# Kernel tuning notes

Measured on AMD Instinct MI355X. Metric: run time of the kernel, lower is better.

The kernel has to match this reference:

```python
import jax, jax.numpy as jnp
import numpy as np

PREV_SIZE = 1024
SIZE = 4096
BATCH = 8192


def setup_inputs() -> dict:
    key = jax.random.key(0)
    k1, k2, k3, k4 = jax.random.split(key, 4)
    return {
        "prev_layer_output": jax.random.normal(k1, (PREV_SIZE, BATCH), dtype=jnp.float32),
        "input_A_weights": jax.random.normal(k2, (SIZE, PREV_SIZE), dtype=jnp.float32),
        "input_B_weights": jax.random.normal(k3, (SIZE, PREV_SIZE), dtype=jnp.float32),
        "table_weights": jax.random.normal(k4, (16, SIZE), dtype=jnp.float32),
    }


def reference(prev_layer_output, input_A_weights, input_B_weights, table_weights):
    # Soft input selection via row-softmax over previous neurons.
    pa = jax.nn.softmax(input_A_weights, axis=1)   # (size, prev_size)
    pb = jax.nn.softmax(input_B_weights, axis=1)   # (size, prev_size)
    pt = jax.nn.softmax(table_weights, axis=0)     # (16, size) softmax over gates

    A = pa @ prev_layer_output                     # (size, batch)
    B = pb @ prev_layer_output                     # (size, batch)
    AB = A * B

    p = pt[:, :, None]                             # (16, size, 1) broadcast over batch
    # Fused weighted sum over the 16 soft logic gates (no (16,size,batch) buffer).
    out = (
        p[1] * AB
        + p[2] * (A - AB)
        + p[3] * A
        + p[4] * (B - AB)
        + p[5] * B
        + p[6] * (A + B - 2.0 * AB)
        + p[7] * (A + B - AB)
        + p[8] * (1.0 - (A + B - AB))
        + p[9] * (1.0 - (A + B - 2.0 * AB))
        + p[10] * (1.0 - B)
        + p[11] * (1.0 - B + AB)
        + p[12] * (1.0 - A)
        + p[13] * (1.0 - A + AB)
        + p[14] * (1.0 - AB)
        + p[15]
    )
    return out
```

## Files before the change

kernel.cpp:

```cpp
#include <hip/hip_runtime.h>
#include <hip/hip_bf16.h>

#define K_DIM 1024
#define M_DIM 4096
#define N_DIM 8192
#define BK 32
#define BM 128
#define BN 128
#define NT 32

#define OFF_A 0
#define OFF_B 8192
#define OFF_P 16384
#define BUF_BYTES 24576

typedef __attribute__((ext_vector_type(8))) __bf16 bf16x8_t;
typedef __attribute__((ext_vector_type(4))) float f32x4;

#define SBAR __builtin_amdgcn_s_barrier()
#define VMCNT0 asm volatile("s_waitcnt vmcnt(0)" ::: "memory")

__device__ inline unsigned short f2bf(float f) {
    unsigned u = __float_as_uint(f);
    u += 0x7FFF + ((u >> 16) & 1);
    return (unsigned short)(u >> 16);
}

__device__ __forceinline__ void gload_lds16(const void* g, void* l) {
    __builtin_amdgcn_global_load_lds(
        (const __attribute__((address_space(1))) unsigned int*)g,
        (__attribute__((address_space(3))) unsigned int*)l, 16, 0, 0);
}

__global__ void dual_softmax_kernel(const float* __restrict__ wa,
                                    const float* __restrict__ wb,
                                    unsigned short* __restrict__ pa,
                                    unsigned short* __restrict__ pb) {
    const int idx = blockIdx.x;
    const float* w = (idx < M_DIM) ? wa : wb;
    unsigned short* o = (idx < M_DIM) ? pa : pb;
    const int row = idx & (M_DIM - 1);
    const int tid = threadIdx.x;
    const float4 v = reinterpret_cast<const float4*>(w + (size_t)row * K_DIM)[tid];
    float m = fmaxf(fmaxf(v.x, v.y), fmaxf(v.z, v.w));
    #pragma unroll
    for (int off = 32; off >= 1; off >>= 1) m = fmaxf(m, __shfl_xor(m, off));
    __shared__ float redm[4];
    __shared__ float reds[4];
    if ((tid & 63) == 0) redm[tid >> 6] = m;
    __syncthreads();
    m = fmaxf(fmaxf(redm[0], redm[1]), fmaxf(redm[2], redm[3]));
    const float e0 = __expf(v.x - m), e1 = __expf(v.y - m);
    const float e2 = __expf(v.z - m), e3 = __expf(v.w - m);
    float s = e0 + e1 + e2 + e3;
    #pragma unroll
    for (int off = 32; off >= 1; off >>= 1) s += __shfl_xor(s, off);
    if ((tid & 63) == 0) reds[tid >> 6] = s;
    __syncthreads();
    s = reds[0] + reds[1] + reds[2] + reds[3];
    const float inv = 1.0f / s;
    ushort4 r;
    r.x = f2bf(e0 * inv); r.y = f2bf(e1 * inv);
    r.z = f2bf(e2 * inv); r.w = f2bf(e3 * inv);
    reinterpret_cast<ushort4*>(o + (size_t)row * K_DIM)[tid] = r;
}

__global__ void transpose_conv_kernel(const float* __restrict__ src,
                                      unsigned short* __restrict__ dst) {
    __shared__ float t[32][33];
    const int n0 = blockIdx.x * 32;
    const int k0 = blockIdx.y * 32;
    const int tx = threadIdx.x, ty = threadIdx.y;
    #pragma unroll
    for (int i = ty; i < 32; i += 8)
        t[i][tx] = src[(size_t)(k0 + i) * N_DIM + n0 + tx];
    __syncthreads();
    #pragma unroll
    for (int i = ty; i < 32; i += 8)
        dst[(size_t)(n0 + i) * K_DIM + k0 + tx] = f2bf(t[tx][i]);
}

__global__ void coef_kernel(const float* __restrict__ tw,
                            float4* __restrict__ coef) {
    const int r = blockIdx.x * 256 + threadIdx.x;
    float p[16];
    float m = -1e30f;
    #pragma unroll
    for (int k = 0; k < 16; ++k) { p[k] = tw[k * M_DIM + r]; m = fmaxf(m, p[k]); }
    float s = 0.f;
    #pragma unroll
    for (int k = 0; k < 16; ++k) { p[k] = __expf(p[k] - m); s += p[k]; }
    const float inv = 1.f / s;
    #pragma unroll
    for (int k = 0; k < 16; ++k) p[k] *= inv;
    const float cA  = p[2]+p[3]+p[6]+p[7]-p[8]-p[9]-p[12]-p[13];
    const float cB  = p[4]+p[5]+p[6]+p[7]-p[8]-p[9]-p[10]-p[11];
    const float cAB = p[1]-p[2]-p[4]-2.f*p[6]-p[7]+p[8]+2.f*p[9]+p[11]+p[13]-p[14];
    const float c0  = p[8]+p[9]+p[10]+p[11]+p[12]+p[13]+p[14]+p[15];
    coef[r] = make_float4(cA, cB, cAB, c0);
}

__global__ __launch_bounds__(256, 2)
void dual_gemm_kernel(const unsigned short* __restrict__ pa,
                      const unsigned short* __restrict__ pb,
                      const unsigned short* __restrict__ pv,
                      const float4* __restrict__ coef,
                      float* __restrict__ out) {
    __shared__ unsigned short lds[2 * BUF_BYTES / 2];

    const int tid = threadIdx.x;
    const int lane = tid & 63;
    const int w = tid >> 6;
    const int wm = w >> 1, wn = w & 1;
    const int bm = blockIdx.y, bn = blockIdx.x;

    const int sub  = lane >> 2;
    const int scol = (lane & 3) ^ ((lane >> 3) & 3);

    const int c0 = 2 * w, c1 = 2 * w + 1;
    const char* sA0 = (const char*)pa + ((size_t)(bm * BM + c0 * 16 + sub) * K_DIM) * 2 + scol * 16;
    const char* sA1 = (const char*)pa + ((size_t)(bm * BM + c1 * 16 + sub) * K_DIM) * 2 + scol * 16;
    const char* sB0 = (const char*)pb + ((size_t)(bm * BM + c0 * 16 + sub) * K_DIM) * 2 + scol * 16;
    const char* sB1 = (const char*)pb + ((size_t)(bm * BM + c1 * 16 + sub) * K_DIM) * 2 + scol * 16;
    const char* sP0 = (const char*)pv + ((size_t)(bn * BN + c0 * 16 + sub) * K_DIM) * 2 + scol * 16;
    const char* sP1 = (const char*)pv + ((size_t)(bn * BN + c1 * 16 + sub) * K_DIM) * 2 + scol * 16;

    const int fr = lane & 15;
    const int fk = lane >> 4;

    int aoff[4], poff[4];
    #pragma unroll
    for (int i = 0; i < 4; ++i) {
        const int ar = wm * 64 + fr + i * 16;
        aoff[i] = ar * 64 + ((fk ^ ((ar >> 1) & 3)) << 4);
        const int pr = wn * 64 + fr + i * 16;
        poff[i] = pr * 64 + ((fk ^ ((pr >> 1) & 3)) << 4);
    }

    f32x4 accA[4][4], accB[4][4];
    const f32x4 z = {0.f, 0.f, 0.f, 0.f};
    #pragma unroll
    for (int i = 0; i < 4; ++i)
        #pragma unroll
        for (int j = 0; j < 4; ++j) { accA[i][j] = z; accB[i][j] = z; }

    #define STAGE_TO(buf_base) do {                                          \
        char* base = (char*)(buf_base);                                      \
        gload_lds16(sA0, base + OFF_A + c0 * 1024);                          \
        gload_lds16(sA1, base + OFF_A + c1 * 1024);                          \
        gload_lds16(sB0, base + OFF_B + c0 * 1024);                          \
        gload_lds16(sB1, base + OFF_B + c1 * 1024);                          \
        gload_lds16(sP0, base + OFF_P + c0 * 1024);                          \
        gload_lds16(sP1, base + OFF_P + c1 * 1024);                          \
        sA0 += BK * 2; sA1 += BK * 2; sB0 += BK * 2; sB1 += BK * 2;          \
        sP0 += BK * 2; sP1 += BK * 2;                                        \
    } while (0)

    char* buf0 = (char*)lds;
    char* buf1 = (char*)lds + BUF_BYTES;

    STAGE_TO(buf0);
    VMCNT0;
    SBAR;

    for (int t = 0; t < NT; ++t) {
        const bool more = (t < NT - 1);
        if (more) STAGE_TO(buf1);

        bf16x8_t af[4], bfv[4], pf[4];
        #pragma unroll
        for (int i = 0; i < 4; ++i) {
            af[i]  = *reinterpret_cast<const bf16x8_t*>(buf0 + OFF_A + aoff[i]);
            bfv[i] = *reinterpret_cast<const bf16x8_t*>(buf0 + OFF_B + aoff[i]);
            pf[i]  = *reinterpret_cast<const bf16x8_t*>(buf0 + OFF_P + poff[i]);
        }

        __builtin_amdgcn_s_setprio(1);
        #pragma unroll
        for (int mi = 0; mi < 4; ++mi)
            #pragma unroll
            for (int ni = 0; ni < 4; ++ni) {
                accA[mi][ni] = __builtin_amdgcn_mfma_f32_16x16x32_bf16(
                    af[mi], pf[ni], accA[mi][ni], 0, 0, 0);
                accB[mi][ni] = __builtin_amdgcn_mfma_f32_16x16x32_bf16(
                    bfv[mi], pf[ni], accB[mi][ni], 0, 0, 0);
            }
        __builtin_amdgcn_s_setprio(0);

        if (more) {
            VMCNT0;
            SBAR;
        }
        char* tmp = buf0; buf0 = buf1; buf1 = tmp;
    }

    const int row_grp = lane >> 4;
    #pragma unroll
    for (int mi = 0; mi < 4; ++mi) {
        #pragma unroll
        for (int ni = 0; ni < 4; ++ni) {
            const int gr0 = bm * BM + wm * 64 + mi * 16 + row_grp * 4;
            const int gc  = bn * BN + wn * 64 + ni * 16 + (lane & 15);
            #pragma unroll
            for (int i = 0; i < 4; ++i) {
                const int r = gr0 + i;
                const float4 cf = coef[r];
                const float av = accA[mi][ni][i];
                const float bv = accB[mi][ni][i];
                out[(size_t)r * N_DIM + gc] =
                    fmaf(cf.z, av * bv, fmaf(cf.x, av, fmaf(cf.y, bv, cf.w)));
            }
        }
    }
}

extern "C" void kernel_launch(void* const* d_in, const int* in_sizes, int n_in,
                              void* d_out, int out_size, void* d_ws, size_t ws_size,
                              hipStream_t stream) {
    const float* prev = (const float*)d_in[0];
    const float* wa   = (const float*)d_in[1];
    const float* wb   = (const float*)d_in[2];
    const float* tw   = (const float*)d_in[3];
    float* out = (float*)d_out;

    char* ws = (char*)d_ws;
    unsigned short* pa = (unsigned short*)ws;
    unsigned short* pb = (unsigned short*)(ws + 8388608);
    unsigned short* pv = (unsigned short*)(ws + 16777216);
    float4* coef       = (float4*)(ws + 33554432);

    dual_softmax_kernel<<<2 * M_DIM, 256, 0, stream>>>(wa, wb, pa, pb);
    transpose_conv_kernel<<<dim3(N_DIM / 32, K_DIM / 32), dim3(32, 8), 0, stream>>>(prev, pv);
    coef_kernel<<<M_DIM / 256, 256, 0, stream>>>(tw, coef);
    dual_gemm_kernel<<<dim3(N_DIM / BN, M_DIM / BM), 256, 0, stream>>>(pa, pb, pv, coef, out);
}
```

Baseline: 164.0 us.

## Load A/B softmax operands directly from global into registers, stage only P in LDS

The A and B weight tiles are no longer staged through LDS. Each wave instead loads its own rows straight from global memory into registers, double-buffered, and only the shared prev-layer tile goes through LDS. This shrinks LDS use from 48KB to 16KB per block and removes LDS read traffic for A/B. The cost is that wm-paired waves load A/B redundantly from global/L2 with less coalesced 16-byte row accesses, and register pressure rises from the extra fragment buffers.

```diff
diff --git a/kernel.cpp b/kernel.cpp
--- a/kernel.cpp
+++ b/kernel.cpp
@@ -9,10 +9,7 @@
 #define BN 128
 #define NT 32
 
-#define OFF_A 0
-#define OFF_B 8192
-#define OFF_P 16384
-#define BUF_BYTES 24576
+#define PBUF_BYTES 8192
 
 typedef __attribute__((ext_vector_type(8))) __bf16 bf16x8_t;
 typedef __attribute__((ext_vector_type(4))) float f32x4;
@@ -106,7 +103,7 @@
                       const unsigned short* __restrict__ pv,
                       const float4* __restrict__ coef,
                       float* __restrict__ out) {
-    __shared__ unsigned short lds[2 * BUF_BYTES / 2];
+    __shared__ unsigned short lds[2 * PBUF_BYTES / 2];
 
     const int tid = threadIdx.x;
     const int lane = tid & 63;
@@ -116,25 +113,22 @@
 
     const int sub  = lane >> 2;
     const int scol = (lane & 3) ^ ((lane >> 3) & 3);
-
     const int c0 = 2 * w, c1 = 2 * w + 1;
-    const char* sA0 = (const char*)pa + ((size_t)(bm * BM + c0 * 16 + sub) * K_DIM) * 2 + scol * 16;
-    const char* sA1 = (const char*)pa + ((size_t)(bm * BM + c1 * 16 + sub) * K_DIM) * 2 + scol * 16;
-    const char* sB0 = (const char*)pb + ((size_t)(bm * BM + c0 * 16 + sub) * K_DIM) * 2 + scol * 16;
-    const char* sB1 = (const char*)pb + ((size_t)(bm * BM + c1 * 16 + sub) * K_DIM) * 2 + scol * 16;
     const char* sP0 = (const char*)pv + ((size_t)(bn * BN + c0 * 16 + sub) * K_DIM) * 2 + scol * 16;
     const char* sP1 = (const char*)pv + ((size_t)(bn * BN + c1 * 16 + sub) * K_DIM) * 2 + scol * 16;
 
+    const unsigned short* gA = pa +
+        (size_t)(bm * BM + wm * 64 + (lane & 15)) * K_DIM + (lane >> 4) * 8;
+    const unsigned short* gB = pb +
+        (size_t)(bm * BM + wm * 64 + (lane & 15)) * K_DIM + (lane >> 4) * 8;
+
     const int fr = lane & 15;
     const int fk = lane >> 4;
-
-    int aoff[4], poff[4];
-    #pragma unroll
-    for (int i = 0; i < 4; ++i) {
-        const int ar = wm * 64 + fr + i * 16;
-        aoff[i] = ar * 64 + ((fk ^ ((ar >> 1) & 3)) << 4);
-        const int pr = wn * 64 + fr + i * 16;
-        poff[i] = pr * 64 + ((fk ^ ((pr >> 1) & 3)) << 4);
+    int poff[4];
+    #pragma unroll
+    for (int ni = 0; ni < 4; ++ni) {
+        const int pr = wn * 64 + fr + ni * 16;
+        poff[ni] = pr * 64 + ((fk ^ ((pr >> 1) & 3)) << 4);
     }
 
     f32x4 accA[4][4], accB[4][4];
@@ -144,55 +138,69 @@
         #pragma unroll
         for (int j = 0; j < 4; ++j) { accA[i][j] = z; accB[i][j] = z; }
 
-    #define STAGE_TO(buf_base) do {                                          \
-        char* base = (char*)(buf_base);                                      \
-        gload_lds16(sA0, base + OFF_A + c0 * 1024);                          \
-        gload_lds16(sA1, base + OFF_A + c1 * 1024);                          \
-        gload_lds16(sB0, base + OFF_B + c0 * 1024);                          \
-        gload_lds16(sB1, base + OFF_B + c1 * 1024);                          \
-        gload_lds16(sP0, base + OFF_P + c0 * 1024);                          \
-        gload_lds16(sP1, base + OFF_P + c1 * 1024);                          \
-        sA0 += BK * 2; sA1 += BK * 2; sB0 += BK * 2; sB1 += BK * 2;          \
+    char* const buf0 = (char*)lds;
+    char* const buf1 = (char*)lds + PBUF_BYTES;
+
+    #define STAGE_P(base) do {                                               \
+        gload_lds16(sP0, (base) + c0 * 1024);                                \
+        gload_lds16(sP1, (base) + c1 * 1024);                                \
         sP0 += BK * 2; sP1 += BK * 2;                                        \
     } while (0)
 
-    char* buf0 = (char*)lds;
-    char* buf1 = (char*)lds + BUF_BYTES;
-
-    STAGE_TO(buf0);
+    #define LOAD_AB(da, db, t) do {                                          \
+        _Pragma("unroll")                                                    \
+        for (int mi = 0; mi < 4; ++mi) {                                     \
+            da[mi] = *reinterpret_cast<const bf16x8_t*>(                     \
+                gA + (size_t)mi * 16 * K_DIM + (t) * BK);                    \
+            db[mi] = *reinterpret_cast<const bf16x8_t*>(                     \
+                gB + (size_t)mi * 16 * K_DIM + (t) * BK);                    \
+        }                                                                    \
+    } while (0)
+
+    #define COMPUTE(da, db, base) do {                                       \
+        bf16x8_t pf[4];                                                      \
+        _Pragma("unroll")                                                    \
+        for (int ni = 0; ni < 4; ++ni)                                       \
+            pf[ni] = *reinterpret_cast<const bf16x8_t*>((base) + poff[ni]);  \
+        __builtin_amdgcn_s_setprio(1);                                       \
+        _Pragma("unroll")                                                    \
+        for (int mi = 0; mi < 4; ++mi)                                       \
+            _Pragma("unroll")                                                \
+            for (int ni = 0; ni < 4; ++ni) {                                 \
+                accA[mi][ni] = __builtin_amdgcn_mfma_f32_16x16x32_bf16(      \
+                    da[mi], pf[ni], accA[mi][ni], 0, 0, 0);                  \
+                accB[mi][ni] = __builtin_amdgcn_mfma_f32_16x16x32_bf16(      \
+                    db[mi], pf[ni], accB[mi][ni], 0, 0, 0);                  \
+            }                                                                \
+        __builtin_amdgcn_s_setprio(0);                                       \
+    } while (0)
+
+    bf16x8_t a0[4], b0[4], a1[4], b1[4];
+
+    LOAD_AB(a0, b0, 0);
+    STAGE_P(buf0);
     VMCNT0;
     SBAR;
 
-    for (int t = 0; t < NT; ++t) {
-        const bool more = (t < NT - 1);
-        if (more) STAGE_TO(buf1);
-
-        bf16x8_t af[4], bfv[4], pf[4];
-        #pragma unroll
-        for (int i = 0; i < 4; ++i) {
-            af[i]  = *reinterpret_cast<const bf16x8_t*>(buf0 + OFF_A + aoff[i]);
-            bfv[i] = *reinterpret_cast<const bf16x8_t*>(buf0 + OFF_B + aoff[i]);
-            pf[i]  = *reinterpret_cast<const bf16x8_t*>(buf0 + OFF_P + poff[i]);
-        }
-
-        __builtin_amdgcn_s_setprio(1);
-        #pragma unroll
-        for (int mi = 0; mi < 4; ++mi)
-            #pragma unroll
-            for (int ni = 0; ni < 4; ++ni) {
-                accA[mi][ni] = __builtin_amdgcn_mfma_f32_16x16x32_bf16(
-                    af[mi], pf[ni], accA[mi][ni], 0, 0, 0);
-                accB[mi][ni] = __builtin_amdgcn_mfma_f32_16x16x32_bf16(
-                    bfv[mi], pf[ni], accB[mi][ni], 0, 0, 0);
-            }
-        __builtin_amdgcn_s_setprio(0);
-
-        if (more) {
-            VMCNT0;
-            SBAR;
-        }
-        char* tmp = buf0; buf0 = buf1; buf1 = tmp;
+    for (int tt = 0; tt < 15; ++tt) {
+        const int t0 = 2 * tt;
+        LOAD_AB(a1, b1, t0 + 1);
+        STAGE_P(buf1);
+        COMPUTE(a0, b0, buf0);
+        VMCNT0;
+        SBAR;
+        LOAD_AB(a0, b0, t0 + 2);
+        STAGE_P(buf0);
+        COMPUTE(a1, b1, buf1);
+        VMCNT0;
+        SBAR;
     }
+    LOAD_AB(a1, b1, 31);
+    STAGE_P(buf1);
+    COMPUTE(a0, b0, buf0);
+    VMCNT0;
+    SBAR;
+    COMPUTE(a1, b1, buf1);
 
     const int row_grp = lane >> 4;
     #pragma unroll
```

Result: slower. 301.3 us (+83.7%).
